# Kernel optimization log

Hardware: AMD Instinct MI355X
Metric: run time of the kernel (lower is better)

Reference implementation:

```python
import jax, jax.numpy as jnp
import numpy as np

B, T, C, H = 2, 2048, 768, 12
HD = C // H  # head dim = 64
EPS = 1e-5


def layer_norm(x, g, b):
    mu = jnp.mean(x, axis=-1, keepdims=True)
    var = jnp.var(x, axis=-1, keepdims=True)
    return (x - mu) * jax.lax.rsqrt(var + EPS) * g + b


def setup_inputs() -> dict:
    key = jax.random.key(0)
    ks = jax.random.split(key, 5)
    s = 0.02
    return {
        "x": jax.random.normal(ks[0], (B, T, C), jnp.float32),
        "ln1_g": jnp.ones((C,), jnp.float32),
        "ln1_b": jnp.zeros((C,), jnp.float32),
        "W_qkv": jax.random.normal(ks[1], (C, 3 * C), jnp.float32) * s,
        "W_attn_proj": jax.random.normal(ks[2], (C, C), jnp.float32) * s,
        "ln2_g": jnp.ones((C,), jnp.float32),
        "ln2_b": jnp.zeros((C,), jnp.float32),
        "W_fc": jax.random.normal(ks[3], (C, 4 * C), jnp.float32) * s,
        "W_mlp_proj": jax.random.normal(ks[4], (4 * C, C), jnp.float32) * s,
    }


def attention(x, W_qkv, W_attn_proj):
    b, t, c = x.shape
    qkv = x @ W_qkv  # [B,T,3C]
    q, k, v = jnp.split(qkv, 3, axis=-1)
    # [B,H,T,HD]
    q = q.reshape(b, t, H, HD).transpose(0, 2, 1, 3)
    k = k.reshape(b, t, H, HD).transpose(0, 2, 1, 3)
    v = v.reshape(b, t, H, HD).transpose(0, 2, 1, 3)
    att = jnp.einsum("bhqd,bhkd->bhqk", q, k) * (1.0 / np.sqrt(HD).astype(np.float32))
    causal = jnp.tril(jnp.ones((t, t), jnp.bool_))
    att = jnp.where(causal, att, jnp.finfo(att.dtype).min)
    att = jax.nn.softmax(att, axis=-1)
    y = jnp.einsum("bhqk,bhkd->bhqd", att, v)
    y = y.transpose(0, 2, 1, 3).reshape(b, t, c)
    return y @ W_attn_proj


def mlp(x, W_fc, W_mlp_proj):
    h = jax.nn.gelu(x @ W_fc, approximate=False)
    return h @ W_mlp_proj


def reference(x, ln1_g, ln1_b, W_qkv, W_attn_proj, ln2_g, ln2_b, W_fc, W_mlp_proj):
    x = x + attention(layer_norm(x, ln1_g, ln1_b), W_qkv, W_attn_proj)
    x = x + mlp(layer_norm(x, ln2_g, ln2_b), W_fc, W_mlp_proj)
    return x
```

## Files before the change

### kernel.cpp

```cpp
#include <hip/hip_runtime.h>
#include <cstdint>
#include <cstddef>

typedef unsigned short u16;
typedef __attribute__((ext_vector_type(4))) float f32x4;
typedef __attribute__((ext_vector_type(8))) short bf16x8;

__device__ __forceinline__ u16 f2bf(float f) {
  unsigned int u = __builtin_bit_cast(unsigned int, f);
  u += 0x7fffu + ((u >> 16) & 1u);
  return (u16)(u >> 16);
}

__device__ __forceinline__ void gl_lds16(const u16* g, u16* lds_base) {
  __builtin_amdgcn_global_load_lds(
      (const __attribute__((address_space(1))) unsigned int*)g,
      (__attribute__((address_space(3))) unsigned int*)lds_base, 16, 0, 0);
}

__global__ __launch_bounds__(256) void transpose_w(const float* __restrict__ src,
                                                   u16* __restrict__ dst,
                                                   int K, int N) {
  __shared__ float tile[32][33];
  int n0 = blockIdx.x * 32, k0 = blockIdx.y * 32;
  int tx = threadIdx.x & 31, ty = threadIdx.x >> 5;
#pragma unroll
  for (int i = 0; i < 4; ++i)
    tile[ty + i * 8][tx] = src[(size_t)(k0 + ty + i * 8) * N + n0 + tx];
  __syncthreads();
#pragma unroll
  for (int i = 0; i < 4; ++i)
    dst[(size_t)(n0 + ty + i * 8) * K + k0 + tx] = f2bf(tile[tx][ty + i * 8]);
}

__global__ __launch_bounds__(256) void transpose_v(const u16* __restrict__ qkvb,
                                                   u16* __restrict__ vt) {
  __shared__ u16 tile[64 * 72];
  int t0 = blockIdx.x * 64;
  int bh = blockIdx.y;
  int b = bh / 12, h = bh % 12;
  int tid = threadIdx.x;
  int c8 = tid & 7, r = tid >> 3;
#pragma unroll
  for (int i = 0; i < 2; ++i) {
    int rr = r + i * 32;
    *(uint4*)&tile[rr * 72 + c8 * 8] =
        *(const uint4*)&qkvb[(size_t)(b * 2048 + t0 + rr) * 2304 + 1536 + h * 64 + c8 * 8];
  }
  __syncthreads();
#pragma unroll
  for (int i = 0; i < 2; ++i) {
    int dr = r + i * 32;
    u16 tmp[8];
#pragma unroll
    for (int j = 0; j < 8; ++j) tmp[j] = tile[(c8 * 8 + j) * 72 + dr];
    *(uint4*)&vt[((size_t)bh * 64 + dr) * 2048 + t0 + c8 * 8] = *(uint4*)tmp;
  }
}

__global__ void zero_counter(unsigned int* c) {
  if (threadIdx.x == 0) *c = 0u;
}

__global__ __launch_bounds__(192) void ln_rows(const float* __restrict__ x,
                                               const float* __restrict__ g,
                                               const float* __restrict__ bb,
                                               u16* __restrict__ out) {
  int row = blockIdx.x;
  int t = threadIdx.x;
  float4 v = *(const float4*)(x + (size_t)row * 768 + t * 4);
  float s = v.x + v.y + v.z + v.w;
  float sq = v.x * v.x + v.y * v.y + v.z * v.z + v.w * v.w;
#pragma unroll
  for (int o = 32; o > 0; o >>= 1) {
    s += __shfl_down(s, o);
    sq += __shfl_down(sq, o);
  }
  __shared__ float ss[3], s2[3];
  int w = t >> 6;
  if ((t & 63) == 0) { ss[w] = s; s2[w] = sq; }
  __syncthreads();
  s = ss[0] + ss[1] + ss[2];
  sq = s2[0] + s2[1] + s2[2];
  float mu = s * (1.f / 768.f);
  float var = sq * (1.f / 768.f) - mu * mu;
  float rs = rsqrtf(var + 1e-5f);
  float4 gv = *(const float4*)(g + t * 4);
  float4 bv = *(const float4*)(bb + t * 4);
  u16 o4[4];
  o4[0] = f2bf((v.x - mu) * rs * gv.x + bv.x);
  o4[1] = f2bf((v.y - mu) * rs * gv.y + bv.y);
  o4[2] = f2bf((v.z - mu) * rs * gv.z + bv.z);
  o4[3] = f2bf((v.w - mu) * rs * gv.w + bv.w);
  *(uint2*)(out + (size_t)row * 768 + t * 4) = *(uint2*)o4;
}

template <int EPI, int TN>
__global__ __launch_bounds__(256, 2) void gemm_bt(const u16* __restrict__ A,
                                                  const u16* __restrict__ BT,
                                                  int M, int N, int K,
                                                  float* __restrict__ outF,
                                                  u16* __restrict__ outB,
                                                  const float* __restrict__ res) {
  constexpr int MT = (TN == 128) ? 4 : 2;
  __shared__ __align__(16) u16 Al[128 * 64];
  __shared__ __align__(16) u16 Bl[TN * 64];
  int tid = threadIdx.x;
  int lane = tid & 63, w = tid >> 6;
  int l16 = lane & 15, quad = lane >> 4;
  int swz = l16 & 7;
  int wm = (TN == 128) ? (w >> 1) : w;
  int wn = (TN == 128) ? (w & 1) : 0;
  size_t rowA0 = (size_t)blockIdx.y * 128;
  size_t rowB0 = (size_t)blockIdx.x * TN;

  f32x4 acc[MT][4] = {};

  for (int k0 = 0; k0 < K; k0 += 64) {
    __syncthreads();
#pragma unroll
    for (int i = 0; i < 4; ++i) {
      int cbase = (i * 4 + w) * 64;
      int chunk = cbase + lane;
      int r = chunk >> 3, c8 = (chunk & 7) ^ (r & 7);
      gl_lds16(&A[(rowA0 + r) * (size_t)K + k0 + c8 * 8], &Al[cbase * 8]);
    }
#pragma unroll
    for (int i = 0; i < TN / 32; ++i) {
      int cbase = (i * 4 + w) * 64;
      int chunk = cbase + lane;
      int r = chunk >> 3, c8 = (chunk & 7) ^ (r & 7);
      gl_lds16(&BT[(rowB0 + r) * (size_t)K + k0 + c8 * 8], &Bl[cbase * 8]);
    }
    __syncthreads();
#pragma unroll
    for (int ks = 0; ks < 2; ++ks) {
      int c = ks * 4 + quad;
      bf16x8 af[MT], bf[4];
#pragma unroll
      for (int mt = 0; mt < MT; ++mt)
        af[mt] = *(const bf16x8*)&Al[(wm * (MT * 16) + mt * 16 + l16) * 64 + (c ^ swz) * 8];
#pragma unroll
      for (int nt = 0; nt < 4; ++nt)
        bf[nt] = *(const bf16x8*)&Bl[(wn * 64 + nt * 16 + l16) * 64 + (c ^ swz) * 8];
#pragma unroll
      for (int mt = 0; mt < MT; ++mt)
#pragma unroll
        for (int nt = 0; nt < 4; ++nt)
          acc[mt][nt] = __builtin_amdgcn_mfma_f32_16x16x32_bf16(af[mt], bf[nt], acc[mt][nt], 0, 0, 0);
    }
  }

#pragma unroll
  for (int mt = 0; mt < MT; ++mt) {
#pragma unroll
    for (int i = 0; i < 4; ++i) {
      size_t row = rowA0 + wm * (MT * 16) + mt * 16 + quad * 4 + i;
#pragma unroll
      for (int nt = 0; nt < 4; ++nt) {
        size_t col = rowB0 + wn * 64 + nt * 16 + l16;
        float v = acc[mt][nt][i];
        if (EPI == 0) {
          outB[row * N + col] = f2bf(v);
        } else if (EPI == 1) {
          outF[row * N + col] = res[row * N + col] + v;
        } else {
          float ge = 0.5f * v * (1.f + erff(v * 0.70710678118654752f));
          outB[row * N + col] = f2bf(ge);
        }
      }
    }
  }
}

__global__ __launch_bounds__(256, 3) void flash_attn(const u16* __restrict__ qkv,
                                                     const u16* __restrict__ vt,
                                                     u16* __restrict__ y,
                                                     unsigned int* __restrict__ ctr) {
  __shared__ __align__(16) u16 Kl[128 * 64];
  __shared__ __align__(16) u16 Vl[64 * 128];
  __shared__ __align__(16) u16 Pl[4][16 * 136];
  __shared__ unsigned int s_unit;

  int tid = threadIdx.x;
  int lane = tid & 63, w = tid >> 6;
  int l16 = lane & 15, quad = lane >> 4;
  int swz = l16 & 7;
  u16* Pw = &Pl[w][0];

  for (;;) {
    __syncthreads();
    if (tid == 0) s_unit = atomicAdd(ctr, 1u);
    __syncthreads();
    unsigned int u = s_unit;
    if (u >= 768u) return;

    int qt = 31 - (int)(u / 24u);
    int bh = (int)(u % 24u);
    int b = bh / 12, h = bh % 12;
    int qw = qt * 64 + w * 16;

    const u16* base = qkv + (size_t)b * 2048 * 2304;
    const u16* vbase = vt + (size_t)bh * 64 * 2048;

    bf16x8 qf0, qf1;
    {
      const u16* qp = base + (size_t)(qw + l16) * 2304 + h * 64 + quad * 8;
      qf0 = *(const bf16x8*)qp;
      qf1 = *(const bf16x8*)(qp + 32);
    }

    f32x4 O[4] = {};
    float l_i[4] = {0.f, 0.f, 0.f, 0.f};

    int nkb = qt / 2 + 1;
    for (int kb = 0; kb < nkb; ++kb) {
      int kt0 = kb << 7;
      __syncthreads();
#pragma unroll
      for (int i = 0; i < 4; ++i) {
        int cbase = (i * 4 + w) * 64;
        int chunk = cbase + lane;
        int r = chunk >> 3, c8 = (chunk & 7) ^ (r & 7);
        gl_lds16(base + (size_t)(kt0 + r) * 2304 + 768 + h * 64 + c8 * 8, &Kl[cbase * 8]);
      }
#pragma unroll
      for (int i = 0; i < 4; ++i) {
        int cbase = (i * 4 + w) * 64;
        int chunk = cbase + lane;
        int r = chunk >> 4, c16 = (chunk & 15) ^ (r & 7);
        gl_lds16(vbase + (size_t)r * 2048 + kt0 + c16 * 8, &Vl[cbase * 8]);
      }
      __syncthreads();

      f32x4 S[8];
#pragma unroll
      for (int nt = 0; nt < 8; ++nt) {
        bf16x8 k0 = *(const bf16x8*)&Kl[(nt * 16 + l16) * 64 + (quad ^ swz) * 8];
        bf16x8 k1 = *(const bf16x8*)&Kl[(nt * 16 + l16) * 64 + ((4 + quad) ^ swz) * 8];
        f32x4 z = {};
        z = __builtin_amdgcn_mfma_f32_16x16x32_bf16(qf0, k0, z, 0, 0, 0);
        S[nt] = __builtin_amdgcn_mfma_f32_16x16x32_bf16(qf1, k1, z, 0, 0, 0);
      }

      const float sc = 0.125f * 1.44269504088896340736f;
      float rowsum[4] = {0.f, 0.f, 0.f, 0.f};
      bool diag = (kb == nkb - 1);
#pragma unroll
      for (int nt = 0; nt < 8; ++nt) {
        int tk = kt0 + nt * 16 + l16;
#pragma unroll
        for (int i = 0; i < 4; ++i) {
          float p = exp2f(S[nt][i] * sc);
          if (diag && tk > qw + quad * 4 + i) p = 0.f;
          rowsum[i] += p;
          Pw[(quad * 4 + i) * 136 + nt * 16 + l16] =
              (u16)(__builtin_bit_cast(unsigned int, p) >> 16);
        }
      }
#pragma unroll
      for (int i = 0; i < 4; ++i) {
#pragma unroll
        for (int o = 1; o < 16; o <<= 1) rowsum[i] += __shfl_xor(rowsum[i], o);
        l_i[i] += rowsum[i];
      }

      asm volatile("s_waitcnt lgkmcnt(0)" ::: "memory");

#pragma unroll
      for (int c = 0; c < 4; ++c) {
        bf16x8 pf = *(const bf16x8*)&Pw[l16 * 136 + c * 32 + quad * 8];
#pragma unroll
        for (int dt = 0; dt < 4; ++dt) {
          bf16x8 vf = *(const bf16x8*)&Vl[(dt * 16 + l16) * 128 + ((c * 4 + quad) ^ swz) * 8];
          O[dt] = __builtin_amdgcn_mfma_f32_16x16x32_bf16(pf, vf, O[dt], 0, 0, 0);
        }
      }
    }

#pragma unroll
    for (int dt = 0; dt < 4; ++dt) {
#pragma unroll
      for (int i = 0; i < 4; ++i) {
        int tq = qw + quad * 4 + i;
        float ov = O[dt][i] / l_i[i];
        y[(size_t)(b * 2048 + tq) * 768 + h * 64 + dt * 16 + l16] = f2bf(ov);
      }
    }
  }
}

extern "C" void kernel_launch(void* const* d_in, const int* in_sizes, int n_in,
                              void* d_out, int out_size, void* d_ws, size_t ws_size,
                              hipStream_t stream) {
  const float* x      = (const float*)d_in[0];
  const float* ln1_g  = (const float*)d_in[1];
  const float* ln1_b  = (const float*)d_in[2];
  const float* W_qkv  = (const float*)d_in[3];
  const float* W_attn = (const float*)d_in[4];
  const float* ln2_g  = (const float*)d_in[5];
  const float* ln2_b  = (const float*)d_in[6];
  const float* W_fc   = (const float*)d_in[7];
  const float* W_mlp  = (const float*)d_in[8];
  float* out = (float*)d_out;

  const int M = 4096;
  char* p = (char*)d_ws;
  auto alloc = [&](size_t bytes) {
    char* r = p;
    p += (bytes + 255) & ~(size_t)255;
    return r;
  };
  u16* wt_qkv  = (u16*)alloc((size_t)2304 * 768 * 2);
  u16* wt_attn = (u16*)alloc((size_t)768 * 768 * 2);
  u16* wt_fc   = (u16*)alloc((size_t)3072 * 768 * 2);
  u16* wt_mlp  = (u16*)alloc((size_t)768 * 3072 * 2);
  u16* xn1     = (u16*)alloc((size_t)M * 768 * 2);
  u16* qkvb    = (u16*)alloc((size_t)M * 2304 * 2);
  u16* yb      = (u16*)alloc((size_t)M * 768 * 2);
  float* x1    = (float*)alloc((size_t)M * 768 * 4);
  u16* xn2     = (u16*)alloc((size_t)M * 768 * 2);
  u16* hb      = (u16*)alloc((size_t)M * 3072 * 2);
  u16* vt      = (u16*)alloc((size_t)24 * 64 * 2048 * 2);
  unsigned int* ctr = (unsigned int*)alloc(256);

  transpose_w<<<dim3(2304 / 32, 768 / 32), 256, 0, stream>>>(W_qkv, wt_qkv, 768, 2304);
  transpose_w<<<dim3(768 / 32, 768 / 32), 256, 0, stream>>>(W_attn, wt_attn, 768, 768);
  transpose_w<<<dim3(3072 / 32, 768 / 32), 256, 0, stream>>>(W_fc, wt_fc, 768, 3072);
  transpose_w<<<dim3(768 / 32, 3072 / 32), 256, 0, stream>>>(W_mlp, wt_mlp, 3072, 768);

  ln_rows<<<M, 192, 0, stream>>>(x, ln1_g, ln1_b, xn1);
  gemm_bt<0, 128><<<dim3(2304 / 128, M / 128), 256, 0, stream>>>(xn1, wt_qkv, M, 2304, 768,
                                                                 nullptr, qkvb, nullptr);
  transpose_v<<<dim3(32, 24), 256, 0, stream>>>(qkvb, vt);
  zero_counter<<<1, 64, 0, stream>>>(ctr);
  flash_attn<<<768, 256, 0, stream>>>(qkvb, vt, yb, ctr);
  gemm_bt<1, 64><<<dim3(768 / 64, M / 128), 256, 0, stream>>>(yb, wt_attn, M, 768, 768,
                                                              x1, nullptr, x);
  ln_rows<<<M, 192, 0, stream>>>(x1, ln2_g, ln2_b, xn2);
  gemm_bt<2, 128><<<dim3(3072 / 128, M / 128), 256, 0, stream>>>(xn2, wt_fc, M, 3072, 768,
                                                                 nullptr, hb, nullptr);
  gemm_bt<1, 64><<<dim3(768 / 64, M / 128), 256, 0, stream>>>(hb, wt_mlp, M, 768, 3072,
                                                              out, nullptr, x1);
}
```

Before: 284.2 us.

## Pre-pack GEMM operands into MFMA fragment layout and drop LDS staging

```diff
diff --git a/kernel.cpp b/kernel.cpp
--- a/kernel.cpp
+++ b/kernel.cpp
@@ -18,19 +18,18 @@
       (__attribute__((address_space(3))) unsigned int*)lds_base, 16, 0, 0);
 }
 
-__global__ __launch_bounds__(256) void transpose_w(const float* __restrict__ src,
-                                                   u16* __restrict__ dst,
-                                                   int K, int N) {
-  __shared__ float tile[32][33];
-  int n0 = blockIdx.x * 32, k0 = blockIdx.y * 32;
-  int tx = threadIdx.x & 31, ty = threadIdx.x >> 5;
-#pragma unroll
-  for (int i = 0; i < 4; ++i)
-    tile[ty + i * 8][tx] = src[(size_t)(k0 + ty + i * 8) * N + n0 + tx];
-  __syncthreads();
-#pragma unroll
-  for (int i = 0; i < 4; ++i)
-    dst[(size_t)(n0 + ty + i * 8) * K + k0 + tx] = f2bf(tile[tx][ty + i * 8]);
+__global__ __launch_bounds__(256) void pack_w(const float* __restrict__ src,
+                                              u16* __restrict__ dst, int K, int N) {
+  int fs = blockIdx.x * 4 + (threadIdx.x >> 6);
+  int lane = threadIdx.x & 63;
+  int nc = K >> 5;
+  int J = fs / nc, C = fs - J * nc;
+  int n = J * 16 + (lane & 15);
+  int k0 = C * 32 + (lane >> 4) * 8;
+  u16 tmp[8];
+#pragma unroll
+  for (int j = 0; j < 8; ++j) tmp[j] = f2bf(src[(size_t)(k0 + j) * N + n]);
+  *(uint4*)&dst[((size_t)fs * 64 + lane) * 8] = *(uint4*)tmp;
 }
 
 __global__ __launch_bounds__(256) void transpose_v(const u16* __restrict__ qkvb,
@@ -92,90 +91,103 @@
   o4[1] = f2bf((v.y - mu) * rs * gv.y + bv.y);
   o4[2] = f2bf((v.z - mu) * rs * gv.z + bv.z);
   o4[3] = f2bf((v.w - mu) * rs * gv.w + bv.w);
-  *(uint2*)(out + (size_t)row * 768 + t * 4) = *(uint2*)o4;
-}
-
-template <int EPI, int TN>
-__global__ __launch_bounds__(256, 2) void gemm_bt(const u16* __restrict__ A,
-                                                  const u16* __restrict__ BT,
-                                                  int M, int N, int K,
+  int I = row >> 4, m16 = row & 15;
+  int C = t >> 3, q8 = (t & 7) >> 1, j = (t & 1) * 4;
+  *(uint2*)&out[(((size_t)I * 24 + C) * 64 + m16 + 16 * q8) * 8 + j] = *(uint2*)o4;
+}
+
+template <int EPI>
+__global__ __launch_bounds__(256, 3) void gemm_fs(const u16* __restrict__ Ap,
+                                                  const u16* __restrict__ Bp,
+                                                  int Mtiles, int N, int K,
                                                   float* __restrict__ outF,
                                                   u16* __restrict__ outB,
-                                                  const float* __restrict__ res) {
-  constexpr int MT = (TN == 128) ? 4 : 2;
-  __shared__ __align__(16) u16 Al[128 * 64];
-  __shared__ __align__(16) u16 Bl[TN * 64];
-  int tid = threadIdx.x;
-  int lane = tid & 63, w = tid >> 6;
+                                                  const float* __restrict__ res,
+                                                  u16* __restrict__ outP, int KP) {
+  __shared__ u16 bounce[(EPI == 2) ? 4 * 64 * 68 : 4];
+  int lane = threadIdx.x & 63, w = threadIdx.x >> 6;
   int l16 = lane & 15, quad = lane >> 4;
-  int swz = l16 & 7;
-  int wm = (TN == 128) ? (w >> 1) : w;
-  int wn = (TN == 128) ? (w & 1) : 0;
-  size_t rowA0 = (size_t)blockIdx.y * 128;
-  size_t rowB0 = (size_t)blockIdx.x * TN;
-
-  f32x4 acc[MT][4] = {};
-
-  for (int k0 = 0; k0 < K; k0 += 64) {
-    __syncthreads();
-#pragma unroll
-    for (int i = 0; i < 4; ++i) {
-      int cbase = (i * 4 + w) * 64;
-      int chunk = cbase + lane;
-      int r = chunk >> 3, c8 = (chunk & 7) ^ (r & 7);
-      gl_lds16(&A[(rowA0 + r) * (size_t)K + k0 + c8 * 8], &Al[cbase * 8]);
+  int tile = blockIdx.x * 4 + w;
+  int J = tile / Mtiles, I = tile - J * Mtiles;
+  int nc = K >> 5;
+  const u16* ap = Ap + ((size_t)I * 4 * nc * 64 + lane) * 8;
+  const u16* bp = Bp + ((size_t)J * 4 * nc * 64 + lane) * 8;
+
+  f32x4 acc[4][4] = {};
+  bf16x8 ac[4], bc[4], an[4], bn[4];
+#pragma unroll
+  for (int mt = 0; mt < 4; ++mt) {
+    ac[mt] = *(const bf16x8*)(ap + (size_t)mt * nc * 512);
+    bc[mt] = *(const bf16x8*)(bp + (size_t)mt * nc * 512);
+  }
+  for (int c = 0; c < nc; ++c) {
+    int c2 = (c + 1 < nc) ? c + 1 : c;
+#pragma unroll
+    for (int mt = 0; mt < 4; ++mt) {
+      an[mt] = *(const bf16x8*)(ap + ((size_t)mt * nc + c2) * 512);
+      bn[mt] = *(const bf16x8*)(bp + ((size_t)mt * nc + c2) * 512);
     }
 #pragma unroll
-    for (int i = 0; i < TN / 32; ++i) {
-      int cbase = (i * 4 + w) * 64;
-      int chunk = cbase + lane;
-      int r = chunk >> 3, c8 = (chunk & 7) ^ (r & 7);
-      gl_lds16(&BT[(rowB0 + r) * (size_t)K + k0 + c8 * 8], &Bl[cbase * 8]);
-    }
-    __syncthreads();
-#pragma unroll
-    for (int ks = 0; ks < 2; ++ks) {
-      int c = ks * 4 + quad;
-      bf16x8 af[MT], bf[4];
-#pragma unroll
-      for (int mt = 0; mt < MT; ++mt)
-        af[mt] = *(const bf16x8*)&Al[(wm * (MT * 16) + mt * 16 + l16) * 64 + (c ^ swz) * 8];
+    for (int mt = 0; mt < 4; ++mt)
 #pragma unroll
       for (int nt = 0; nt < 4; ++nt)
-        bf[nt] = *(const bf16x8*)&Bl[(wn * 64 + nt * 16 + l16) * 64 + (c ^ swz) * 8];
-#pragma unroll
-      for (int mt = 0; mt < MT; ++mt)
+        acc[mt][nt] = __builtin_amdgcn_mfma_f32_16x16x32_bf16(ac[mt], bc[nt], acc[mt][nt], 0, 0, 0);
+#pragma unroll
+    for (int mt = 0; mt < 4; ++mt) { ac[mt] = an[mt]; bc[mt] = bn[mt]; }
+  }
+
+  int m0 = I * 64, n0 = J * 64;
+  if (EPI == 0) {
+#pragma unroll
+    for (int mt = 0; mt < 4; ++mt)
+#pragma unroll
+      for (int i = 0; i < 4; ++i) {
+        size_t row = m0 + mt * 16 + quad * 4 + i;
 #pragma unroll
         for (int nt = 0; nt < 4; ++nt)
-          acc[mt][nt] = __builtin_amdgcn_mfma_f32_16x16x32_bf16(af[mt], bf[nt], acc[mt][nt], 0, 0, 0);
-    }
-  }
-
-#pragma unroll
-  for (int mt = 0; mt < MT; ++mt) {
-#pragma unroll
-    for (int i = 0; i < 4; ++i) {
-      size_t row = rowA0 + wm * (MT * 16) + mt * 16 + quad * 4 + i;
-#pragma unroll
-      for (int nt = 0; nt < 4; ++nt) {
-        size_t col = rowB0 + wn * 64 + nt * 16 + l16;
-        float v = acc[mt][nt][i];
-        if (EPI == 0) {
-          outB[row * N + col] = f2bf(v);
-        } else if (EPI == 1) {
-          outF[row * N + col] = res[row * N + col] + v;
-        } else {
+          outB[row * N + n0 + nt * 16 + l16] = f2bf(acc[mt][nt][i]);
+      }
+  } else if (EPI == 1) {
+#pragma unroll
+    for (int mt = 0; mt < 4; ++mt)
+#pragma unroll
+      for (int i = 0; i < 4; ++i) {
+        size_t row = m0 + mt * 16 + quad * 4 + i;
+#pragma unroll
+        for (int nt = 0; nt < 4; ++nt) {
+          size_t col = n0 + nt * 16 + l16;
+          outF[row * N + col] = res[row * N + col] + acc[mt][nt][i];
+        }
+      }
+  } else {
+    u16* bw = &bounce[w * 64 * 68];
+#pragma unroll
+    for (int mt = 0; mt < 4; ++mt)
+#pragma unroll
+      for (int nt = 0; nt < 4; ++nt)
+#pragma unroll
+        for (int i = 0; i < 4; ++i) {
+          float v = acc[mt][nt][i];
           float ge = 0.5f * v * (1.f + erff(v * 0.70710678118654752f));
-          outB[row * N + col] = f2bf(ge);
+          bw[(mt * 16 + quad * 4 + i) * 68 + nt * 16 + l16] = f2bf(ge);
         }
-      }
-    }
+    asm volatile("s_waitcnt lgkmcnt(0)" ::: "memory");
+    int ncp = KP >> 5;
+#pragma unroll
+    for (int mt2 = 0; mt2 < 4; ++mt2)
+#pragma unroll
+      for (int cc = 0; cc < 2; ++cc) {
+        uint4 vv = *(const uint4*)&bw[(mt2 * 16 + l16) * 68 + cc * 32 + quad * 8];
+        size_t I2 = (size_t)(m0 >> 4) + mt2;
+        size_t Cg = (size_t)(n0 >> 5) + cc;
+        *(uint4*)&outP[((I2 * ncp + Cg) * 64 + lane) * 8] = vv;
+      }
   }
 }
 
 __global__ __launch_bounds__(256, 3) void flash_attn(const u16* __restrict__ qkv,
                                                      const u16* __restrict__ vt,
-                                                     u16* __restrict__ y,
+                                                     u16* __restrict__ yp,
                                                      unsigned int* __restrict__ ctr) {
   __shared__ __align__(16) u16 Kl[128 * 64];
   __shared__ __align__(16) u16 Vl[64 * 128];
@@ -279,13 +291,16 @@
     }
 
 #pragma unroll
-    for (int dt = 0; dt < 4; ++dt) {
-#pragma unroll
-      for (int i = 0; i < 4; ++i) {
-        int tq = qw + quad * 4 + i;
-        float ov = O[dt][i] / l_i[i];
-        y[(size_t)(b * 2048 + tq) * 768 + h * 64 + dt * 16 + l16] = f2bf(ov);
-      }
+    for (int dt = 0; dt < 4; ++dt)
+#pragma unroll
+      for (int i = 0; i < 4; ++i)
+        Pw[(quad * 4 + i) * 136 + dt * 16 + l16] = f2bf(O[dt][i] / l_i[i]);
+    asm volatile("s_waitcnt lgkmcnt(0)" ::: "memory");
+    int I = (b * 2048 + qw) >> 4;
+#pragma unroll
+    for (int cc = 0; cc < 2; ++cc) {
+      uint4 vv = *(const uint4*)&Pw[l16 * 136 + cc * 32 + quad * 8];
+      *(uint4*)&yp[(((size_t)I * 24 + (h * 2 + cc)) * 64 + lane) * 8] = vv;
     }
   }
 }
@@ -311,35 +326,35 @@
     p += (bytes + 255) & ~(size_t)255;
     return r;
   };
-  u16* wt_qkv  = (u16*)alloc((size_t)2304 * 768 * 2);
-  u16* wt_attn = (u16*)alloc((size_t)768 * 768 * 2);
-  u16* wt_fc   = (u16*)alloc((size_t)3072 * 768 * 2);
-  u16* wt_mlp  = (u16*)alloc((size_t)768 * 3072 * 2);
-  u16* xn1     = (u16*)alloc((size_t)M * 768 * 2);
-  u16* qkvb    = (u16*)alloc((size_t)M * 2304 * 2);
-  u16* yb      = (u16*)alloc((size_t)M * 768 * 2);
-  float* x1    = (float*)alloc((size_t)M * 768 * 4);
-  u16* xn2     = (u16*)alloc((size_t)M * 768 * 2);
-  u16* hb      = (u16*)alloc((size_t)M * 3072 * 2);
-  u16* vt      = (u16*)alloc((size_t)24 * 64 * 2048 * 2);
+  u16* wq   = (u16*)alloc((size_t)2304 * 768 * 2);
+  u16* wa   = (u16*)alloc((size_t)768 * 768 * 2);
+  u16* wf   = (u16*)alloc((size_t)3072 * 768 * 2);
+  u16* wm   = (u16*)alloc((size_t)768 * 3072 * 2);
+  u16* xn1  = (u16*)alloc((size_t)M * 768 * 2);
+  u16* qkvb = (u16*)alloc((size_t)M * 2304 * 2);
+  u16* ybp  = (u16*)alloc((size_t)M * 768 * 2);
+  float* x1 = (float*)alloc((size_t)M * 768 * 4);
+  u16* xn2  = (u16*)alloc((size_t)M * 768 * 2);
+  u16* hbp  = (u16*)alloc((size_t)M * 3072 * 2);
+  u16* vt   = (u16*)alloc((size_t)24 * 64 * 2048 * 2);
   unsigned int* ctr = (unsigned int*)alloc(256);
 
-  transpose_w<<<dim3(2304 / 32, 768 / 32), 256, 0, stream>>>(W_qkv, wt_qkv, 768, 2304);
-  transpose_w<<<dim3(768 / 32, 768 / 32), 256, 0, stream>>>(W_attn, wt_attn, 768, 768);
-  transpose_w<<<dim3(3072 / 32, 768 / 32), 256, 0, stream>>>(W_fc, wt_fc, 768, 3072);
-  transpose_w<<<dim3(768 / 32, 3072 / 32), 256, 0, stream>>>(W_mlp, wt_mlp, 3072, 768);
+  pack_w<<<(2304 / 16) * (768 / 32) / 4, 256, 0, stream>>>(W_qkv, wq, 768, 2304);
+  pack_w<<<(768 / 16) * (768 / 32) / 4, 256, 0, stream>>>(W_attn, wa, 768, 768);
+  pack_w<<<(3072 / 16) * (768 / 32) / 4, 256, 0, stream>>>(W_fc, wf, 768, 3072);
+  pack_w<<<(768 / 16) * (3072 / 32) / 4, 256, 0, stream>>>(W_mlp, wm, 3072, 768);
 
   ln_rows<<<M, 192, 0, stream>>>(x, ln1_g, ln1_b, xn1);
-  gemm_bt<0, 128><<<dim3(2304 / 128, M / 128), 256, 0, stream>>>(xn1, wt_qkv, M, 2304, 768,
-                                                                 nullptr, qkvb, nullptr);
+  gemm_fs<0><<<576, 256, 0, stream>>>(xn1, wq, 64, 2304, 768,
+                                      nullptr, qkvb, nullptr, nullptr, 0);
   transpose_v<<<dim3(32, 24), 256, 0, stream>>>(qkvb, vt);
   zero_counter<<<1, 64, 0, stream>>>(ctr);
-  flash_attn<<<768, 256, 0, stream>>>(qkvb, vt, yb, ctr);
-  gemm_bt<1, 64><<<dim3(768 / 64, M / 128), 256, 0, stream>>>(yb, wt_attn, M, 768, 768,
-                                                              x1, nullptr, x);
+  flash_attn<<<768, 256, 0, stream>>>(qkvb, vt, ybp, ctr);
+  gemm_fs<1><<<192, 256, 0, stream>>>(ybp, wa, 64, 768, 768,
+                                      x1, nullptr, x, nullptr, 0);
   ln_rows<<<M, 192, 0, stream>>>(x1, ln2_g, ln2_b, xn2);
-  gemm_bt<2, 128><<<dim3(3072 / 128, M / 128), 256, 0, stream>>>(xn2, wt_fc, M, 3072, 768,
-                                                                 nullptr, hb, nullptr);
-  gemm_bt<1, 64><<<dim3(768 / 64, M / 128), 256, 0, stream>>>(hb, wt_mlp, M, 768, 3072,
-                                                              out, nullptr, x1);
-}
+  gemm_fs<2><<<768, 256, 0, stream>>>(xn2, wf, 64, 3072, 768,
+                                      nullptr, nullptr, nullptr, hbp, 3072);
+  gemm_fs<1><<<192, 256, 0, stream>>>(hbp, wm, 64, 768, 3072,
+                                      out, nullptr, x1, nullptr, 0);
+}
```

Result: slower. 395.3 us (+39.1%).
